# Kernel optimization log

Hardware: AMD Instinct MI355X
Metric: run time of the kernel (lower is better)

The kernel has to match this reference:

```python
import jax, jax.numpy as jnp
import numpy as np

S, H, I, E, TOP_K = 8192, 2048, 2048, 8, 2


def setup_inputs() -> dict:
    key = jax.random.key(0)
    k0, k1, k2, k3 = jax.random.split(key, 4)
    scale = 1.0 / np.sqrt(H)
    return {
        "hidden_states": jax.random.normal(k0, (S, H), dtype=jnp.float32),
        "w_gate": jax.random.normal(k1, (E, H), dtype=jnp.float32) * scale,
        "w1": jax.random.normal(k2, (E, 2 * I, H), dtype=jnp.float32) * scale,
        "w2": jax.random.normal(k3, (E, H, I), dtype=jnp.float32) * (1.0 / np.sqrt(I)),
        "top_k": TOP_K,
    }


def reference(hidden_states, w_gate, w1, w2, top_k):
    # Router: logits -> float32 softmax -> top-k -> renormalize
    router_logits = hidden_states @ w_gate.T                      # [S, E]
    probs = jax.nn.softmax(router_logits.astype(jnp.float32), axis=-1)
    top_p, top_i = jax.lax.top_k(probs, top_k)                    # [S, k]
    top_p = top_p / jnp.sum(top_p, axis=-1, keepdims=True)

    n_tok, n_exp = probs.shape
    # Dense combine weights [S, E]; zero for non-selected experts.
    combine = jnp.zeros((n_tok, n_exp), dtype=probs.dtype)
    combine = combine.at[jnp.arange(n_tok)[:, None], top_i].add(top_p)

    inter = w2.shape[2]
    out = jnp.zeros_like(hidden_states)
    # Loop over the small fixed expert set; masked-combine gives exact
    # fused_moe semantics (scatter-combine of weighted expert outputs).
    for e in range(n_exp):
        gu = hidden_states @ w1[e].T                              # [S, 2I]
        gate, up = gu[:, :inter], gu[:, inter:]
        h = jax.nn.silu(gate) * up                                # SiluAndMul
        out = out + combine[:, e:e + 1].astype(hidden_states.dtype) * (h @ w2[e].T)
    return out, router_logits
```

## Files before the change

### kernel.cpp

```cpp
#include <hip/hip_runtime.h>
#include <hip/hip_bf16.h>
#include <stdint.h>

#define S_TOK 8192
#define H_DIM 2048
#define I_DIM 2048
#define E_NUM 8

typedef __attribute__((ext_vector_type(4))) float f32x4;
typedef __attribute__((ext_vector_type(8))) short bf16x8;
typedef __attribute__((ext_vector_type(8))) unsigned short u16x8;

#define MFMA16(a, b, c) __builtin_amdgcn_mfma_f32_16x16x32_bf16((a), (b), (c), 0, 0, 0)

__device__ __forceinline__ unsigned short f2bf(float f) {
    unsigned int u = __float_as_uint(f);
    unsigned int r = (u + 0x7FFFu + ((u >> 16) & 1u)) >> 16;
    return (unsigned short)r;
}
__device__ __forceinline__ float bf2f(unsigned short u) {
    return __uint_as_float((unsigned int)u << 16);
}

__device__ __forceinline__ void cvt8(const float* __restrict__ s, unsigned short* __restrict__ d) {
    float4 v0 = *(const float4*)s;
    float4 v1 = *(const float4*)(s + 4);
    u16x8 o;
    o[0] = f2bf(v0.x); o[1] = f2bf(v0.y); o[2] = f2bf(v0.z); o[3] = f2bf(v0.w);
    o[4] = f2bf(v1.x); o[5] = f2bf(v1.y); o[6] = f2bf(v1.z); o[7] = f2bf(v1.w);
    *(u16x8*)d = o;
}

__device__ __forceinline__ void async_copy16(void* lds, const void* g) {
    __builtin_amdgcn_global_load_lds(
        (const __attribute__((address_space(1))) void*)(uintptr_t)g,
        (__attribute__((address_space(3))) void*)(uintptr_t)lds,
        16, 0, 0);
}

__device__ __forceinline__ int xcd_swizzle(int bid, int nwg) {
    int cpx = nwg >> 3;
    return (bid & 7) * cpx + (bid >> 3);
}

__global__ void cvt_kernel(const float* __restrict__ src, unsigned short* __restrict__ dst, long n) {
    long i0 = ((long)blockIdx.x * blockDim.x + threadIdx.x) * 8;
    long stride = (long)gridDim.x * blockDim.x * 8;
    for (long i = i0; i < n; i += stride) cvt8(src + i, dst + i);
}

template<int HALF>
__device__ __forceinline__ void cvt_w1_half_body(const float* __restrict__ src,
                                                 unsigned short* __restrict__ dst,
                                                 long i0, long stride) {
    const long CH = 1L << 21;
    const long TOT = (long)E_NUM * 2 * CH;
    for (long j = i0; j < TOT; j += stride) {
        long e = j >> 22;
        long piece = (j >> 21) & 1;
        long off = j & (CH - 1);
        long g = (e << 23) + ((piece * 2 + HALF) << 21) + off;
        cvt8(src + g, dst + g);
    }
}

__global__ void router_kernel(const float* __restrict__ hs, const float* __restrict__ wg,
                              float* __restrict__ logits,
                              unsigned int* __restrict__ tchoice, float* __restrict__ twgt,
                              unsigned short* __restrict__ hsb,
                              const float* __restrict__ w1src, unsigned short* __restrict__ w1dst,
                              int cvt_blks) {
    if ((int)blockIdx.x >= S_TOK) {
        long i0 = ((long)((int)blockIdx.x - S_TOK) * blockDim.x + threadIdx.x) * 8;
        long stride = (long)cvt_blks * blockDim.x * 8;
        cvt_w1_half_body<0>(w1src, w1dst, i0, stride);
        return;
    }
    int t = blockIdx.x;
    int tid = threadIdx.x;
    const float* hrow = hs + (size_t)t * H_DIM;
    float4 h0 = *(const float4*)(hrow + tid * 8);
    float4 h1 = *(const float4*)(hrow + tid * 8 + 4);
    u16x8 o;
    o[0] = f2bf(h0.x); o[1] = f2bf(h0.y); o[2] = f2bf(h0.z); o[3] = f2bf(h0.w);
    o[4] = f2bf(h1.x); o[5] = f2bf(h1.y); o[6] = f2bf(h1.z); o[7] = f2bf(h1.w);
    *(u16x8*)(hsb + (size_t)t * H_DIM + tid * 8) = o;

    float p[E_NUM];
#pragma unroll
    for (int e = 0; e < E_NUM; ++e) {
        const float* w = wg + (size_t)e * H_DIM + tid * 8;
        float4 w0 = *(const float4*)(w);
        float4 w1v = *(const float4*)(w + 4);
        p[e] = h0.x * w0.x + h0.y * w0.y + h0.z * w0.z + h0.w * w0.w +
               h1.x * w1v.x + h1.y * w1v.y + h1.z * w1v.z + h1.w * w1v.w;
    }
#pragma unroll
    for (int e = 0; e < E_NUM; ++e)
#pragma unroll
        for (int d = 32; d > 0; d >>= 1) p[e] += __shfl_xor(p[e], d, 64);

    __shared__ float red[4][E_NUM];
    int wave = tid >> 6, lane = tid & 63;
    if (lane == 0) {
#pragma unroll
        for (int e = 0; e < E_NUM; ++e) red[wave][e] = p[e];
    }
    __syncthreads();
    if (tid == 0) {
        float l[E_NUM];
#pragma unroll
        for (int e = 0; e < E_NUM; ++e) l[e] = red[0][e] + red[1][e] + red[2][e] + red[3][e];
#pragma unroll
        for (int e = 0; e < E_NUM; ++e) logits[(size_t)t * E_NUM + e] = l[e];
        int i1 = 0;
#pragma unroll
        for (int e = 1; e < E_NUM; ++e) if (l[e] > l[i1]) i1 = e;
        int i2 = (i1 == 0) ? 1 : 0;
#pragma unroll
        for (int e = 0; e < E_NUM; ++e) if (e != i1 && l[e] > l[i2]) i2 = e;
        float b = __expf(l[i2] - l[i1]);
        tchoice[t] = (unsigned)i1 | ((unsigned)i2 << 4);
        twgt[t] = 1.0f / (1.0f + b);
    }
}

__global__ __launch_bounds__(1024) void scan_kernel(
    const unsigned int* __restrict__ tchoice, const float* __restrict__ twgt,
    int* __restrict__ cnt, int* __restrict__ off,
    int* __restrict__ tok_of, float* __restrict__ wgt_of,
    unsigned int* __restrict__ slot_of) {
    __shared__ int lcnt[E_NUM][1024];
    __shared__ int tot[E_NUM];
    int tid = threadIdx.x;
    unsigned int ch[8];
    int c[E_NUM];
#pragma unroll
    for (int e = 0; e < E_NUM; ++e) c[e] = 0;
#pragma unroll
    for (int k = 0; k < 8; ++k) {
        ch[k] = tchoice[tid * 8 + k];
        c[ch[k] & 15]++;
        c[(ch[k] >> 4) & 15]++;
    }
#pragma unroll
    for (int e = 0; e < E_NUM; ++e) lcnt[e][tid] = c[e];
    __syncthreads();
    int wave = tid >> 6, lane = tid & 63;
    if (wave < E_NUM) {
        int base = 0;
        for (int chk = 0; chk < 16; ++chk) {
            int v = lcnt[wave][chk * 64 + lane];
            int inc = v;
#pragma unroll
            for (int d = 1; d < 64; d <<= 1) {
                int u = __shfl_up(inc, d, 64);
                if (lane >= d) inc += u;
            }
            lcnt[wave][chk * 64 + lane] = base + inc - v;
            base += __shfl(inc, 63, 64);
        }
        if (lane == 0) tot[wave] = base;
    }
    __syncthreads();
    if (tid == 0) {
        int s = 0;
#pragma unroll
        for (int e = 0; e < E_NUM; ++e) { off[e] = s; cnt[e] = tot[e]; s += tot[e]; }
    }
    __syncthreads();
#pragma unroll
    for (int e = 0; e < E_NUM; ++e) c[e] = lcnt[e][tid];
#pragma unroll
    for (int k = 0; k < 8; ++k) {
        int t = tid * 8 + k;
        int i1 = ch[k] & 15, i2 = (ch[k] >> 4) & 15;
        float wA = twgt[t];
        int s1 = c[i1]++;
        int s2 = c[i2]++;
        tok_of[i1 * S_TOK + s1] = t; wgt_of[i1 * S_TOK + s1] = wA;
        tok_of[i2 * S_TOK + s2] = t; wgt_of[i2 * S_TOK + s2] = 1.0f - wA;
        slot_of[2 * t]     = ((unsigned)i1 << 20) | (unsigned)s1;
        slot_of[2 * t + 1] = ((unsigned)i2 << 20) | (unsigned)s2;
    }
}

__global__ void combine_kernel(const unsigned short* __restrict__ pbuf,
                               const unsigned int* __restrict__ slot_of,
                               const int* __restrict__ off, float* __restrict__ out) {
    int t = blockIdx.x, tid = threadIdx.x;
    unsigned int a = slot_of[2 * t], b = slot_of[2 * t + 1];
    size_t ra = (size_t)(off[a >> 20] + (int)(a & 0xFFFFFu));
    size_t rb = (size_t)(off[b >> 20] + (int)(b & 0xFFFFFu));
    const unsigned short* pa = pbuf + ra * H_DIM + tid * 8;
    const unsigned short* pb = pbuf + rb * H_DIM + tid * 8;
    ushort4 a0 = *(const ushort4*)pa, a1 = *(const ushort4*)(pa + 4);
    ushort4 b0 = *(const ushort4*)pb, b1 = *(const ushort4*)(pb + 4);
    float4 r0, r1;
    r0.x = bf2f(a0.x) + bf2f(b0.x); r0.y = bf2f(a0.y) + bf2f(b0.y);
    r0.z = bf2f(a0.z) + bf2f(b0.z); r0.w = bf2f(a0.w) + bf2f(b0.w);
    r1.x = bf2f(a1.x) + bf2f(b1.x); r1.y = bf2f(a1.y) + bf2f(b1.y);
    r1.z = bf2f(a1.z) + bf2f(b1.z); r1.w = bf2f(a1.w) + bf2f(b1.w);
    float* op = out + (size_t)t * H_DIM + tid * 8;
    *(float4*)op = r0;
    *(float4*)(op + 4) = r1;
}

template<int IS_G1>
__global__ __launch_bounds__(512, 2) void moe_gemm_kernel(
    const unsigned short* __restrict__ A_src, const unsigned short* __restrict__ W,
    const int* __restrict__ cnt, const int* __restrict__ off,
    const int* __restrict__ tok_of, const float* __restrict__ wgt_of,
    unsigned short* __restrict__ dst,
    const float* __restrict__ cvt_src, unsigned short* __restrict__ cvt_dst,
    long cvt_n, int gemm_grid, int cvt_blks, int nt_base, int cvt_mode) {
    if ((int)blockIdx.x >= gemm_grid) {
        long i0 = ((long)((int)blockIdx.x - gemm_grid) * blockDim.x + threadIdx.x) * 8;
        long stride = (long)cvt_blks * blockDim.x * 8;
        if (cvt_mode == 2) {
            cvt_w1_half_body<1>(cvt_src, cvt_dst, i0, stride);
        } else if (cvt_mode == 1) {
            for (long i = i0; i < cvt_n; i += stride) cvt8(cvt_src + i, cvt_dst + i);
        }
        return;
    }
    int bx = xcd_swizzle(blockIdx.x, gemm_grid);
    int nt = nt_base + bx / (E_NUM * 32);
    int rr = bx % (E_NUM * 32);
    int e = rr / 32;
    int mt = rr % 32;
    int C = cnt[e];
    if (mt * 256 >= C) return;
    int O = off[e];

    __shared__ __align__(16) char ldsA[2][32768];
    __shared__ __align__(16) char ldsB[2][32768];

    int tid = threadIdx.x;
    int wave = tid >> 6, lane = tid & 63;
    int wr = wave >> 2, wc = wave & 3;

    const char* aptr[4];
#pragma unroll
    for (int q = 0; q < 4; ++q) {
        int row = q * 64 + wave * 8 + (lane >> 3);
        int cu = (lane & 7) ^ (row & 7);
        int grow = mt * 256 + row; if (grow > C - 1) grow = C - 1;
        size_t arow = IS_G1 ? (size_t)tok_of[e * S_TOK + grow] : (size_t)(O + grow);
        aptr[q] = (const char*)(A_src + arow * 2048 + cu * 8);
    }
    const char* bptr[4];
#pragma unroll
    for (int j = 0; j < 4; ++j) {
        int lrow = j * 64 + wave * 8 + (lane >> 3);
        int cu = (lane & 7) ^ (lrow & 7);
        int np = lrow >> 7, wcg = (lrow >> 5) & 3, rem = lrow & 31;
        int tbrow = wcg * 64 + np * 32 + rem;
        size_t brow;
        if (IS_G1) {
            int jj = tbrow & 63, wq = tbrow >> 6;
            if (jj < 32) brow = (size_t)(nt * 128 + wq * 32 + jj);
            else         brow = (size_t)I_DIM + nt * 128 + wq * 32 + (jj - 32);
            brow += (size_t)e * (2 * I_DIM);
        } else {
            brow = (size_t)e * H_DIM + nt * 256 + tbrow;
        }
        bptr[j] = (const char*)(W + brow * 2048 + cu * 8);
    }

    int aoff[8][2], boff[4][2];
#pragma unroll
    for (int m = 0; m < 8; ++m)
#pragma unroll
        for (int ks = 0; ks < 2; ++ks) {
            int row = wr * 128 + m * 16 + (lane & 15);
            int cu = ks * 4 + (lane >> 4);
            aoff[m][ks] = row * 128 + ((cu ^ (row & 7)) * 16);
        }
#pragma unroll
    for (int n = 0; n < 4; ++n)
#pragma unroll
        for (int ks = 0; ks < 2; ++ks) {
            int lrow = (n >> 1) * 128 + wc * 32 + (n & 1) * 16 + (lane & 15);
            int cu = ks * 4 + (lane >> 4);
            boff[n][ks] = lrow * 128 + ((cu ^ (lrow & 7)) * 16);
        }

    f32x4 acc[8][4];
#pragma unroll
    for (int m = 0; m < 8; ++m)
#pragma unroll
        for (int n = 0; n < 4; ++n)
#pragma unroll
            for (int q = 0; q < 4; ++q) acc[m][n][q] = 0.0f;

    auto gA = [&](int q, int T, int buf) {
        async_copy16(ldsA[buf] + q * 8192 + wave * 1024, aptr[q] + T * 128);
    };
    auto gB = [&](int j, int T, int buf) {
        async_copy16(ldsB[buf] + j * 8192 + wave * 1024, bptr[j] + T * 128);
    };

    gA(0, 0, 0); gA(1, 0, 0); gA(2, 0, 0); gA(3, 0, 0);
    gB(0, 0, 0); gB(1, 0, 0); gB(2, 0, 0); gB(3, 0, 0);
    gA(0, 1, 1); gA(1, 1, 1); gA(2, 1, 1); gA(3, 1, 1);
    asm volatile("s_waitcnt vmcnt(4)" ::: "memory");
    __builtin_amdgcn_s_barrier();

    bf16x8 ar[8][2], br[4][2];
    int cur = 0;
#pragma unroll 2
    for (int T = 0; T < 32; ++T) {
        int nxt = cur ^ 1;
        int TA = (T + 2 < 32) ? T + 2 : 31;
        int TB = (T + 1 < 32) ? T + 1 : 31;
#pragma unroll
        for (int n = 0; n < 2; ++n)
#pragma unroll
            for (int ks = 0; ks < 2; ++ks)
                br[n][ks] = *(const bf16x8*)(ldsB[cur] + boff[n][ks]);
#pragma unroll
        for (int m = 0; m < 8; ++m)
#pragma unroll
            for (int ks = 0; ks < 2; ++ks)
                ar[m][ks] = *(const bf16x8*)(ldsA[cur] + aoff[m][ks]);
#pragma unroll
        for (int n = 2; n < 4; ++n)
#pragma unroll
            for (int ks = 0; ks < 2; ++ks)
                br[n][ks] = *(const bf16x8*)(ldsB[cur] + boff[n][ks]);
        gB(0, TB, nxt); gB(1, TB, nxt); gB(2, TB, nxt); gB(3, TB, nxt);
        __builtin_amdgcn_s_setprio(1);
#pragma unroll
        for (int m = 0; m < 4; ++m)
#pragma unroll
            for (int n = 0; n < 2; ++n) {
                acc[m][n] = MFMA16(ar[m][0], br[n][0], acc[m][n]);
                acc[m][n] = MFMA16(ar[m][1], br[n][1], acc[m][n]);
            }
        __builtin_amdgcn_s_setprio(0);
        __builtin_amdgcn_s_barrier();
        gA(0, TA, cur); gA(2, TA, cur);
        __builtin_amdgcn_s_setprio(1);
#pragma unroll
        for (int m = 4; m < 8; ++m)
#pragma unroll
            for (int n = 0; n < 2; ++n) {
                acc[m][n] = MFMA16(ar[m][0], br[n][0], acc[m][n]);
                acc[m][n] = MFMA16(ar[m][1], br[n][1], acc[m][n]);
            }
        __builtin_amdgcn_s_setprio(0);
        __builtin_amdgcn_s_barrier();
        gA(1, TA, cur); gA(3, TA, cur);
        __builtin_amdgcn_s_setprio(1);
#pragma unroll
        for (int m = 0; m < 8; ++m)
#pragma unroll
            for (int n = 0; n < 2; ++n) {
                acc[m][n + 2] = MFMA16(ar[m][0], br[n + 2][0], acc[m][n + 2]);
                acc[m][n + 2] = MFMA16(ar[m][1], br[n + 2][1], acc[m][n + 2]);
            }
        __builtin_amdgcn_s_setprio(0);
        asm volatile("s_waitcnt vmcnt(4)" ::: "memory");
        __builtin_amdgcn_s_barrier();
        cur = nxt;
    }

    if (IS_G1) {
#pragma unroll
        for (int m = 0; m < 8; ++m)
#pragma unroll
            for (int q = 0; q < 4; ++q) {
                int row = mt * 256 + wr * 128 + m * 16 + (lane >> 4) * 4 + q;
                if (row < C) {
                    float wgt = wgt_of[e * S_TOK + row];
                    unsigned short* hp = dst + (size_t)(O + row) * I_DIM +
                                         nt * 128 + wc * 32 + (lane & 15);
#pragma unroll
                    for (int n = 0; n < 2; ++n) {
                        float g = acc[m][n][q];
                        float u = acc[m][n + 2][q];
                        float hv = (g / (1.0f + __expf(-g))) * u * wgt;
                        hp[n * 16] = f2bf(hv);
                    }
                }
            }
    } else {
#pragma unroll
        for (int m = 0; m < 8; ++m)
#pragma unroll
            for (int q = 0; q < 4; ++q) {
                int row = mt * 256 + wr * 128 + m * 16 + (lane >> 4) * 4 + q;
                if (row < C) {
                    unsigned short* pp = dst + (size_t)(O + row) * H_DIM +
                                         nt * 256 + wc * 64 + (lane & 15);
#pragma unroll
                    for (int n = 0; n < 4; ++n)
                        pp[n * 16] = f2bf(acc[m][n][q]);
                }
            }
    }
}

extern "C" void kernel_launch(void* const* d_in, const int* in_sizes, int n_in,
                              void* d_out, int out_size, void* d_ws, size_t ws_size,
                              hipStream_t stream) {
    const float* hs = (const float*)d_in[0];
    const float* wg = (const float*)d_in[1];
    const float* w1 = (const float*)d_in[2];
    const float* w2 = (const float*)d_in[3];

    float* out = (float*)d_out;
    float* logits = out + (size_t)S_TOK * H_DIM;

    char* ws = (char*)d_ws;
    int* cnt = (int*)ws;
    int* off = (int*)(ws + 256);
    int* tok_of = (int*)(ws + 512);
    float* wgt_of = (float*)(ws + 512 + (size_t)E_NUM * S_TOK * 4);
    unsigned int* slot_of = (unsigned int*)(ws + 512 + (size_t)E_NUM * S_TOK * 8);
    unsigned int* tchoice = (unsigned int*)(ws + 512 + (size_t)E_NUM * S_TOK * 8 + (size_t)S_TOK * 8);
    float* twgt = (float*)(ws + 512 + (size_t)E_NUM * S_TOK * 8 + (size_t)S_TOK * 12);
    size_t o = 512 + (size_t)E_NUM * S_TOK * 8 + (size_t)S_TOK * 16;
    o = (o + 4095) & ~(size_t)4095;
    unsigned short* hsb = (unsigned short*)(ws + o);  o += (size_t)S_TOK * H_DIM * 2;
    unsigned short* wxb = (unsigned short*)(ws + o);  o += (size_t)E_NUM * 2 * I_DIM * H_DIM * 2;
    unsigned short* hbuf = (unsigned short*)(ws + o); o += (size_t)S_TOK * 2 * I_DIM * 2;
    size_t o_w2 = o;
    size_t need_fused = o_w2 + (size_t)E_NUM * H_DIM * I_DIM * 2;
    bool fused = (ws_size >= need_fused);

    const long W1_N = (long)E_NUM * 2 * I_DIM * H_DIM;
    const long W2_N = (long)E_NUM * H_DIM * I_DIM;
    const int GRID = E_NUM * 32 * 8;
    const int CVT_BLKS = 1024;

    if (fused) {
        unsigned short* w2b = (unsigned short*)(ws + o_w2);
        unsigned short* pbuf = wxb;
        router_kernel<<<S_TOK + CVT_BLKS, 256, 0, stream>>>(
            hs, wg, logits, tchoice, twgt, hsb, w1, wxb, CVT_BLKS);
        scan_kernel<<<1, 1024, 0, stream>>>(tchoice, twgt, cnt, off, tok_of, wgt_of, slot_of);
        moe_gemm_kernel<1><<<GRID + CVT_BLKS, 512, 0, stream>>>(
            hsb, wxb, cnt, off, tok_of, wgt_of, hbuf,
            w1, wxb, 0, GRID, CVT_BLKS, 0, 2);
        moe_gemm_kernel<1><<<GRID + CVT_BLKS, 512, 0, stream>>>(
            hsb, wxb, cnt, off, tok_of, wgt_of, hbuf,
            w2, w2b, W2_N, GRID, CVT_BLKS, 8, 1);
        moe_gemm_kernel<0><<<GRID, 512, 0, stream>>>(
            hbuf, w2b, cnt, off, tok_of, wgt_of, pbuf,
            nullptr, nullptr, 0, GRID, 0, 0, 0);
        combine_kernel<<<S_TOK, 256, 0, stream>>>(pbuf, slot_of, off, out);
    } else {
        unsigned short* w2b = wxb;
        unsigned short* pbuf = wxb + (size_t)E_NUM * H_DIM * I_DIM;
        router_kernel<<<S_TOK, 256, 0, stream>>>(
            hs, wg, logits, tchoice, twgt, hsb, nullptr, nullptr, 1);
        scan_kernel<<<1, 1024, 0, stream>>>(tchoice, twgt, cnt, off, tok_of, wgt_of, slot_of);
        cvt_kernel<<<4096, 256, 0, stream>>>(w1, wxb, W1_N);
        moe_gemm_kernel<1><<<GRID, 512, 0, stream>>>(
            hsb, wxb, cnt, off, tok_of, wgt_of, hbuf, nullptr, nullptr, 0, GRID, 0, 0, 0);
        moe_gemm_kernel<1><<<GRID, 512, 0, stream>>>(
            hsb, wxb, cnt, off, tok_of, wgt_of, hbuf, nullptr, nullptr, 0, GRID, 0, 8, 0);
        cvt_kernel<<<4096, 256, 0, stream>>>(w2, w2b, W2_N);
        moe_gemm_kernel<0><<<GRID, 512, 0, stream>>>(
            hbuf, w2b, cnt, off, tok_of, wgt_of, pbuf, nullptr, nullptr, 0, GRID, 0, 0, 0);
        combine_kernel<<<S_TOK, 256, 0, stream>>>(pbuf, slot_of, off, out);
    }
}
```

Measured before the change: 616.2 us.

## Switch grouped GEMM from 16x16x32 to 32x32x16 bf16 MFMA tiles

Replaces the 16x16x32 MFMA inner product with 32x32x16 MFMA, which changes the per-wave fragment layout, the LDS read offsets, the B-row permutation used to pair gate and up columns, and the epilogue row/column mapping. Larger MFMA tiles cut LDS fragment reads per FLOP and instruction count. The main loop also collapses from three MFMA phases with staggered A prefetches to two phases, issuing all four A prefetches at once. Register pressure and the scheduling of global loads against MFMA issue change as a result.

```diff
diff --git a/kernel.cpp b/kernel.cpp
--- a/kernel.cpp
+++ b/kernel.cpp
@@ -8,10 +8,11 @@
 #define E_NUM 8
 
 typedef __attribute__((ext_vector_type(4))) float f32x4;
+typedef __attribute__((ext_vector_type(16))) float f32x16;
 typedef __attribute__((ext_vector_type(8))) short bf16x8;
 typedef __attribute__((ext_vector_type(8))) unsigned short u16x8;
 
-#define MFMA16(a, b, c) __builtin_amdgcn_mfma_f32_16x16x32_bf16((a), (b), (c), 0, 0, 0)
+#define MFMA32(a, b, c) __builtin_amdgcn_mfma_f32_32x32x16_bf16((a), (b), (c), 0, 0, 0)
 
 __device__ __forceinline__ unsigned short f2bf(float f) {
     unsigned int u = __float_as_uint(f);
@@ -254,45 +255,42 @@
     for (int j = 0; j < 4; ++j) {
         int lrow = j * 64 + wave * 8 + (lane >> 3);
         int cu = (lane & 7) ^ (lrow & 7);
-        int np = lrow >> 7, wcg = (lrow >> 5) & 3, rem = lrow & 31;
-        int tbrow = wcg * 64 + np * 32 + rem;
         size_t brow;
         if (IS_G1) {
-            int jj = tbrow & 63, wq = tbrow >> 6;
-            if (jj < 32) brow = (size_t)(nt * 128 + wq * 32 + jj);
-            else         brow = (size_t)I_DIM + nt * 128 + wq * 32 + (jj - 32);
-            brow += (size_t)e * (2 * I_DIM);
+            int wcg = lrow >> 6, n = (lrow >> 5) & 1, r = lrow & 31;
+            brow = (size_t)e * (2 * I_DIM) + (size_t)(n ? I_DIM : 0) +
+                   (size_t)(nt * 128 + wcg * 32 + r);
         } else {
-            brow = (size_t)e * H_DIM + nt * 256 + tbrow;
+            brow = (size_t)e * H_DIM + nt * 256 + lrow;
         }
         bptr[j] = (const char*)(W + brow * 2048 + cu * 8);
     }
 
-    int aoff[8][2], boff[4][2];
-#pragma unroll
-    for (int m = 0; m < 8; ++m)
-#pragma unroll
-        for (int ks = 0; ks < 2; ++ks) {
-            int row = wr * 128 + m * 16 + (lane & 15);
-            int cu = ks * 4 + (lane >> 4);
-            aoff[m][ks] = row * 128 + ((cu ^ (row & 7)) * 16);
+    int aoff[4][4], boff[2][4];
+#pragma unroll
+    for (int m = 0; m < 4; ++m)
+#pragma unroll
+        for (int s = 0; s < 4; ++s) {
+            int row = wr * 128 + m * 32 + (lane & 31);
+            int cu = s * 2 + (lane >> 5);
+            aoff[m][s] = row * 128 + ((cu ^ (row & 7)) * 16);
         }
 #pragma unroll
-    for (int n = 0; n < 4; ++n)
-#pragma unroll
-        for (int ks = 0; ks < 2; ++ks) {
-            int lrow = (n >> 1) * 128 + wc * 32 + (n & 1) * 16 + (lane & 15);
-            int cu = ks * 4 + (lane >> 4);
-            boff[n][ks] = lrow * 128 + ((cu ^ (lrow & 7)) * 16);
+    for (int n = 0; n < 2; ++n)
+#pragma unroll
+        for (int s = 0; s < 4; ++s) {
+            int lrow = wc * 64 + n * 32 + (lane & 31);
+            int cu = s * 2 + (lane >> 5);
+            boff[n][s] = lrow * 128 + ((cu ^ (lrow & 7)) * 16);
         }
 
-    f32x4 acc[8][4];
-#pragma unroll
-    for (int m = 0; m < 8; ++m)
-#pragma unroll
-        for (int n = 0; n < 4; ++n)
-#pragma unroll
-            for (int q = 0; q < 4; ++q) acc[m][n][q] = 0.0f;
+    f32x16 acc[4][2];
+#pragma unroll
+    for (int m = 0; m < 4; ++m)
+#pragma unroll
+        for (int n = 0; n < 2; ++n)
+#pragma unroll
+            for (int q = 0; q < 16; ++q) acc[m][n][q] = 0.0f;
 
     auto gA = [&](int q, int T, int buf) {
         async_copy16(ldsA[buf] + q * 8192 + wave * 1024, aptr[q] + T * 128);
@@ -307,7 +305,7 @@
     asm volatile("s_waitcnt vmcnt(4)" ::: "memory");
     __builtin_amdgcn_s_barrier();
 
-    bf16x8 ar[8][2], br[4][2];
+    bf16x8 ar[4][4], br[2][4];
     int cur = 0;
 #pragma unroll 2
     for (int T = 0; T < 32; ++T) {
@@ -317,86 +315,65 @@
 #pragma unroll
         for (int n = 0; n < 2; ++n)
 #pragma unroll
-            for (int ks = 0; ks < 2; ++ks)
-                br[n][ks] = *(const bf16x8*)(ldsB[cur] + boff[n][ks]);
-#pragma unroll
-        for (int m = 0; m < 8; ++m)
-#pragma unroll
-            for (int ks = 0; ks < 2; ++ks)
-                ar[m][ks] = *(const bf16x8*)(ldsA[cur] + aoff[m][ks]);
-#pragma unroll
-        for (int n = 2; n < 4; ++n)
-#pragma unroll
-            for (int ks = 0; ks < 2; ++ks)
-                br[n][ks] = *(const bf16x8*)(ldsB[cur] + boff[n][ks]);
+            for (int s = 0; s < 4; ++s)
+                br[n][s] = *(const bf16x8*)(ldsB[cur] + boff[n][s]);
+#pragma unroll
+        for (int m = 0; m < 4; ++m)
+#pragma unroll
+            for (int s = 0; s < 4; ++s)
+                ar[m][s] = *(const bf16x8*)(ldsA[cur] + aoff[m][s]);
         gB(0, TB, nxt); gB(1, TB, nxt); gB(2, TB, nxt); gB(3, TB, nxt);
         __builtin_amdgcn_s_setprio(1);
 #pragma unroll
-        for (int m = 0; m < 4; ++m)
-#pragma unroll
-            for (int n = 0; n < 2; ++n) {
-                acc[m][n] = MFMA16(ar[m][0], br[n][0], acc[m][n]);
-                acc[m][n] = MFMA16(ar[m][1], br[n][1], acc[m][n]);
-            }
+        for (int m = 0; m < 2; ++m)
+#pragma unroll
+            for (int n = 0; n < 2; ++n)
+#pragma unroll
+                for (int s = 0; s < 4; ++s)
+                    acc[m][n] = MFMA32(ar[m][s], br[n][s], acc[m][n]);
         __builtin_amdgcn_s_setprio(0);
         __builtin_amdgcn_s_barrier();
-        gA(0, TA, cur); gA(2, TA, cur);
+        gA(0, TA, cur); gA(1, TA, cur); gA(2, TA, cur); gA(3, TA, cur);
         __builtin_amdgcn_s_setprio(1);
 #pragma unroll
-        for (int m = 4; m < 8; ++m)
-#pragma unroll
-            for (int n = 0; n < 2; ++n) {
-                acc[m][n] = MFMA16(ar[m][0], br[n][0], acc[m][n]);
-                acc[m][n] = MFMA16(ar[m][1], br[n][1], acc[m][n]);
-            }
-        __builtin_amdgcn_s_setprio(0);
-        __builtin_amdgcn_s_barrier();
-        gA(1, TA, cur); gA(3, TA, cur);
-        __builtin_amdgcn_s_setprio(1);
-#pragma unroll
-        for (int m = 0; m < 8; ++m)
-#pragma unroll
-            for (int n = 0; n < 2; ++n) {
-                acc[m][n + 2] = MFMA16(ar[m][0], br[n + 2][0], acc[m][n + 2]);
-                acc[m][n + 2] = MFMA16(ar[m][1], br[n + 2][1], acc[m][n + 2]);
-            }
+        for (int m = 2; m < 4; ++m)
+#pragma unroll
+            for (int n = 0; n < 2; ++n)
+#pragma unroll
+                for (int s = 0; s < 4; ++s)
+                    acc[m][n] = MFMA32(ar[m][s], br[n][s], acc[m][n]);
         __builtin_amdgcn_s_setprio(0);
         asm volatile("s_waitcnt vmcnt(4)" ::: "memory");
         __builtin_amdgcn_s_barrier();
         cur = nxt;
     }
 
+    int colj = lane & 31, rhi = (lane >> 5) * 4;
     if (IS_G1) {
 #pragma unroll
-        for (int m = 0; m < 8; ++m)
-#pragma unroll
-            for (int q = 0; q < 4; ++q) {
-                int row = mt * 256 + wr * 128 + m * 16 + (lane >> 4) * 4 + q;
+        for (int m = 0; m < 4; ++m)
+#pragma unroll
+            for (int r = 0; r < 16; ++r) {
+                int row = mt * 256 + wr * 128 + m * 32 + (r & 3) + 8 * (r >> 2) + rhi;
                 if (row < C) {
                     float wgt = wgt_of[e * S_TOK + row];
-                    unsigned short* hp = dst + (size_t)(O + row) * I_DIM +
-                                         nt * 128 + wc * 32 + (lane & 15);
-#pragma unroll
-                    for (int n = 0; n < 2; ++n) {
-                        float g = acc[m][n][q];
-                        float u = acc[m][n + 2][q];
-                        float hv = (g / (1.0f + __expf(-g))) * u * wgt;
-                        hp[n * 16] = f2bf(hv);
-                    }
+                    float g = acc[m][0][r];
+                    float u = acc[m][1][r];
+                    float hv = (g / (1.0f + __expf(-g))) * u * wgt;
+                    dst[(size_t)(O + row) * I_DIM + nt * 128 + wc * 32 + colj] = f2bf(hv);
                 }
             }
     } else {
 #pragma unroll
-        for (int m = 0; m < 8; ++m)
-#pragma unroll
-            for (int q = 0; q < 4; ++q) {
-                int row = mt * 256 + wr * 128 + m * 16 + (lane >> 4) * 4 + q;
+        for (int m = 0; m < 4; ++m)
+#pragma unroll
+            for (int r = 0; r < 16; ++r) {
+                int row = mt * 256 + wr * 128 + m * 32 + (r & 3) + 8 * (r >> 2) + rhi;
                 if (row < C) {
                     unsigned short* pp = dst + (size_t)(O + row) * H_DIM +
-                                         nt * 256 + wc * 64 + (lane & 15);
-#pragma unroll
-                    for (int n = 0; n < 4; ++n)
-                        pp[n * 16] = f2bf(acc[m][n][q]);
+                                         nt * 256 + wc * 64 + colj;
+                    pp[0] = f2bf(acc[m][0][r]);
+                    pp[32] = f2bf(acc[m][1][r]);
                 }
             }
     }
```

Result: slower. 842.2 us (+36.7%).
